# Kernel tuning notes

Hardware: AMD Instinct MI355X
Metric: run time of the kernel (lower is better)

The kernel has to match this reference:

```python
import jax, jax.numpy as jnp
import numpy as np

GROUP_SIZE = 64  # quantization group size along in_features (K)


def setup_inputs() -> dict:
    key = jax.random.key(0)
    k1, k2, k3, k4, k5 = jax.random.split(key, 5)
    M, K, N = 32, 8192, 8192
    num_groups = K // GROUP_SIZE
    x = jax.random.normal(k1, (M, K), dtype=jnp.float32)
    # packed int4 weights: two nibbles per byte along K -> [N, K//2]
    packed_weight = jax.random.randint(k2, (N, K // 2), 0, 256, dtype=jnp.int32)
    scales = jax.random.uniform(k3, (N, num_groups), dtype=jnp.float32) * 0.02 + 1e-3
    zeros = jax.random.uniform(k4, (N, num_groups), dtype=jnp.float32) * 15.0
    bias_param = jax.random.normal(k5, (N,), dtype=jnp.float32)
    return {"x": x, "packed_weight": packed_weight, "scales": scales,
            "zeros": zeros, "bias_param": bias_param}


def reference(x, packed_weight, scales, zeros, bias_param):
    # x: [M, K] float; packed_weight: [N, K//2] int (uint8 semantics)
    # scales/zeros: [N, num_groups]; bias_param: [N]
    K = x.shape[-1]
    k = jnp.arange(K)
    shift = (k % 2) * 4                     # low nibble for even k, high for odd
    # unpack int4: q[n, k] in [0, 15]
    q = (packed_weight[:, k // 2] >> shift[None, :]) & 15   # [N, K]
    gidx = k // GROUP_SIZE                                  # [K]
    # group-wise dequant: (q - zero) * scale
    w = (q.astype(jnp.float32) - zeros[:, gidx]) * scales[:, gidx]  # [N, K]
    out = jnp.einsum('mk,nk->mn', x, w) + bias_param[None, :]        # [M, N]
    return out
```

## Files before the change

### kernel.cpp

```cpp
#include <hip/hip_runtime.h>
#include <hip/hip_bf16.h>


#define KK 8192
#define NN 8192
#define KP 4096
#define NG 128
#define BN 16
#define KSPLIT 2
#define KSW 32
#define NKS 256

typedef __attribute__((ext_vector_type(8))) short short8;
typedef __attribute__((ext_vector_type(4))) float floatx4;

__device__ __forceinline__ unsigned pack_bf16x2(float lo, float hi) {
    union { __hip_bfloat162 h; unsigned u; } c;
    c.h = __float22bfloat162_rn(make_float2(lo, hi));
    return c.u;
}

__global__ void prep_kernel(const float* __restrict__ x, const float* __restrict__ bias,
                            ushort* __restrict__ xb, float* __restrict__ out,
                            int xconv_blocks)
{
    const int bx = blockIdx.x;
    if (bx < xconv_blocks) {
        const int tid = bx * 256 + threadIdx.x;
        const int l   = tid & 63;
        const int ks  = (tid >> 6) & 255;
        const int mt  = tid >> 14;
        const int m   = (l & 15) + 16 * mt;
        const int kb  = ks * 32 + (l >> 4) * 8;
        const float* src = x + (size_t)m * KK + kb;
        const float4 a = *(const float4*)(src);
        const float4 b = *(const float4*)(src + 4);
        *(uint4*)(xb + (size_t)tid * 8) =
            make_uint4(pack_bf16x2(a.x, a.y), pack_bf16x2(a.z, a.w),
                       pack_bf16x2(b.x, b.y), pack_bf16x2(b.z, b.w));
    } else {
        const int f4 = (bx - xconv_blocks) * 256 + threadIdx.x;
        const int n4 = f4 & (NN / 4 - 1);
        const float4 b4 = ((const float4*)bias)[n4];
        ((float4*)out)[f4] = b4;
    }
}

template<bool USE_WS>
__global__ __launch_bounds__(256, 4)
void gptq_mfma_kernel(const int*   __restrict__ pw,
                      const float* __restrict__ scales,
                      const float* __restrict__ zeros,
                      const ushort* __restrict__ xb,
                      const float* __restrict__ x,
                      float* __restrict__ out)
{
    __shared__ float s_lds[64][BN + 1];
    __shared__ float z_lds[64][BN + 1];
    __shared__ float red[4][2][256];

    const int tid  = threadIdx.x;
    const int lane = tid & 63;
    const int wave = tid >> 6;
    const int kh   = blockIdx.x & (KSPLIT - 1);
    const int n0   = (blockIdx.x >> 1) * BN;
    const int g0   = kh * 64;

    {
        const int r  = tid >> 4;
        const int gb = (tid & 15) * 4;
        const float4 s4 = *(const float4*)(scales + (size_t)(n0 + r) * NG + g0 + gb);
        const float4 z4 = *(const float4*)(zeros  + (size_t)(n0 + r) * NG + g0 + gb);
        s_lds[gb + 0][r] = s4.x; s_lds[gb + 1][r] = s4.y;
        s_lds[gb + 2][r] = s4.z; s_lds[gb + 3][r] = s4.w;
        z_lds[gb + 0][r] = z4.x; z_lds[gb + 1][r] = z4.y;
        z_lds[gb + 2][r] = z4.z; z_lds[gb + 3][r] = z4.w;
    }
    __syncthreads();

    const int nl = lane & 15;
    const int kq = lane >> 4;
    const int* pwp = pw + (size_t)(n0 + nl) * KP + kq * 4;
    const uint4* xfp = (const uint4*)xb;
    const int ks0 = kh * 128 + wave * KSW;

    const int xm0 = nl;
    const int xkq = kq * 8;

    auto load_xfrag = [&](int mt, int ks) -> uint4 {
        if (USE_WS) {
            return xfp[(size_t)(mt * NKS + ks) * 64 + lane];
        } else {
            const float* src = x + (size_t)(xm0 + 16 * mt) * KK + ks * 32 + xkq;
            const float4 a = *(const float4*)(src);
            const float4 b = *(const float4*)(src + 4);
            return make_uint4(pack_bf16x2(a.x, a.y), pack_bf16x2(a.z, a.w),
                              pack_bf16x2(b.x, b.y), pack_bf16x2(b.z, b.w));
        }
    };

    floatx4 acc0 = {0.f, 0.f, 0.f, 0.f};
    floatx4 acc1 = {0.f, 0.f, 0.f, 0.f};

    int4  pwb[4];
    uint4 x0b[4], x1b[4];

#pragma unroll
    for (int i = 0; i < 3; ++i) {
        const int ks = ks0 + i;
        pwb[i] = *(const int4*)(pwp + ks * 16);
        x0b[i] = load_xfrag(0, ks);
        x1b[i] = load_xfrag(1, ks);
    }

#pragma unroll 4
    for (int i = 0; i < KSW; ++i) {
        const int slot = i & 3;
        if (i + 3 < KSW) {
            const int ks = ks0 + i + 3;
            const int ps = (i + 3) & 3;
            pwb[ps] = *(const int4*)(pwp + ks * 16);
            x0b[ps] = load_xfrag(0, ks);
            x1b[ps] = load_xfrag(1, ks);
        }
        const int gl  = (wave * KSW + i) >> 1;
        const float sc = s_lds[gl][nl];
        const float zs = -z_lds[gl][nl] * sc;

        union { uint4 v; short8 s; } bf;
        const int4 p = pwb[slot];
        bf.v.x = pack_bf16x2(fmaf((float)(p.x & 15), sc, zs),
                             fmaf((float)((p.x >> 4) & 15), sc, zs));
        bf.v.y = pack_bf16x2(fmaf((float)(p.y & 15), sc, zs),
                             fmaf((float)((p.y >> 4) & 15), sc, zs));
        bf.v.z = pack_bf16x2(fmaf((float)(p.z & 15), sc, zs),
                             fmaf((float)((p.z >> 4) & 15), sc, zs));
        bf.v.w = pack_bf16x2(fmaf((float)(p.w & 15), sc, zs),
                             fmaf((float)((p.w >> 4) & 15), sc, zs));

        union { uint4 v; short8 s; } a0, a1;
        a0.v = x0b[slot];
        a1.v = x1b[slot];
        acc0 = __builtin_amdgcn_mfma_f32_16x16x32_bf16(a0.s, bf.s, acc0, 0, 0, 0);
        acc1 = __builtin_amdgcn_mfma_f32_16x16x32_bf16(a1.s, bf.s, acc1, 0, 0, 0);
    }

#pragma unroll
    for (int r = 0; r < 4; ++r) {
        const int row = kq * 4 + r;
        red[wave][0][row * 16 + nl] = acc0[r];
        red[wave][1][row * 16 + nl] = acc1[r];
    }
    __syncthreads();

#pragma unroll
    for (int i = 0; i < 2; ++i) {
        const int e   = i * 256 + tid;
        const int mt  = e >> 8;
        const int idx = e & 255;
        const float s = red[0][mt][idx] + red[1][mt][idx] + red[2][mt][idx] + red[3][mt][idx];
        const int row = idx >> 4, col = idx & 15;
        atomicAdd(out + (size_t)(mt * 16 + row) * NN + n0 + col, s);
    }
}

extern "C" void kernel_launch(void* const* d_in, const int* in_sizes, int n_in,
                              void* d_out, int out_size, void* d_ws, size_t ws_size,
                              hipStream_t stream) {
    const float* x      = (const float*)d_in[0];
    const int*   pw     = (const int*)  d_in[1];
    const float* scales = (const float*)d_in[2];
    const float* zeros  = (const float*)d_in[3];
    const float* bias   = (const float*)d_in[4];
    float* out = (float*)d_out;

    const size_t need = (size_t)32768 * 16;
    const bool use_ws = (d_ws != nullptr && ws_size >= need);

    if (use_ws) {
        ushort* xb = (ushort*)d_ws;
        prep_kernel<<<128 + 256, 256, 0, stream>>>(x, bias, xb, out, 128);
        gptq_mfma_kernel<true><<<512 * KSPLIT, 256, 0, stream>>>(pw, scales, zeros, xb, x, out);
    } else {
        prep_kernel<<<256, 256, 0, stream>>>(x, bias, nullptr, out, 0);
        gptq_mfma_kernel<false><<<512 * KSPLIT, 256, 0, stream>>>(pw, scales, zeros,
                                                                  (const ushort*)nullptr, x, out);
    }
}
```

Before: 214.6 us.

## Stage weights and activations into LDS via async global_load_lds triple buffering

Replaces the register-prefetch main kernel with one that streams packed weights and bf16 activation fragments into per-wave LDS ring buffers using global_load_lds, with manual vmcnt waits giving a three-deep pipeline. The weight tile is XOR-swizzled to avoid bank conflicts. Scales and zero-offsets now live in registers instead of LDS. A cheaper bit-trick bf16 rounding with v_perm replaces the library pack. The aim is to hide memory latency and free VGPRs, at the cost of lower occupancy (launch bounds 2) and a large LDS footprint.

```diff
diff --git a/kernel.cpp b/kernel.cpp
--- a/kernel.cpp
+++ b/kernel.cpp
@@ -1,5 +1,6 @@
 #include <hip/hip_runtime.h>
 #include <hip/hip_bf16.h>
+#include <stdint.h>
 
 
 #define KK 8192
@@ -10,14 +11,31 @@
 #define KSPLIT 2
 #define KSW 32
 #define NKS 256
+#define NCH 16
+#define BUFB 6144
+#define WREG (3 * BUFB)
 
 typedef __attribute__((ext_vector_type(8))) short short8;
 typedef __attribute__((ext_vector_type(4))) float floatx4;
+typedef const __attribute__((address_space(1))) void* gbl_t;
+typedef __attribute__((address_space(3))) void* lds_t;
+
+__device__ __forceinline__ void async16(const void* g, void* l) {
+    __builtin_amdgcn_global_load_lds((gbl_t)(uintptr_t)g, (lds_t)(uintptr_t)l, 16, 0, 0);
+}
 
 __device__ __forceinline__ unsigned pack_bf16x2(float lo, float hi) {
     union { __hip_bfloat162 h; unsigned u; } c;
     c.h = __float22bfloat162_rn(make_float2(lo, hi));
     return c.u;
+}
+
+__device__ __forceinline__ unsigned dq2(int q, float sc, float zs) {
+    float lo = fmaf((float)(q & 15),        sc, zs);
+    float hi = fmaf((float)((q >> 4) & 15), sc, zs);
+    unsigned ua = __float_as_uint(lo); ua += 0x7fffu + ((ua >> 16) & 1u);
+    unsigned ub = __float_as_uint(hi); ub += 0x7fffu + ((ub >> 16) & 1u);
+    return __builtin_amdgcn_perm(ub, ua, 0x07060302);
 }
 
 __global__ void prep_kernel(const float* __restrict__ x, const float* __restrict__ bias,
@@ -41,19 +59,131 @@
     } else {
         const int f4 = (bx - xconv_blocks) * 256 + threadIdx.x;
         const int n4 = f4 & (NN / 4 - 1);
-        const float4 b4 = ((const float4*)bias)[n4];
-        ((float4*)out)[f4] = b4;
-    }
-}
-
-template<bool USE_WS>
+        ((float4*)out)[f4] = ((const float4*)bias)[n4];
+    }
+}
+
+__global__ __launch_bounds__(256, 2)
+void gptq_mfma_lds(const int*   __restrict__ pw,
+                   const float* __restrict__ scales,
+                   const float* __restrict__ zeros,
+                   const ushort* __restrict__ xb,
+                   float* __restrict__ out)
+{
+    __shared__ uint4 smem4[4 * WREG / 16];
+    uint8_t* smem = (uint8_t*)smem4;
+
+    const int tid  = threadIdx.x;
+    const int lane = tid & 63;
+    const int wave = tid >> 6;
+    const int kh   = blockIdx.x & (KSPLIT - 1);
+    const int n0   = (blockIdx.x >> 1) * BN;
+    const int nl   = lane & 15;
+    const int kq   = lane >> 4;
+    const int ks0  = kh * 128 + wave * KSW;
+    const int g0   = ks0 >> 1;
+
+    float scr[16], zsr[16];
+    {
+        const float* sp = scales + (size_t)(n0 + nl) * NG + g0;
+        const float* zp = zeros  + (size_t)(n0 + nl) * NG + g0;
+#pragma unroll
+        for (int i = 0; i < 4; ++i) {
+            const float4 s4 = *(const float4*)(sp + i * 4);
+            const float4 z4 = *(const float4*)(zp + i * 4);
+            scr[i*4+0] = s4.x; zsr[i*4+0] = -z4.x * s4.x;
+            scr[i*4+1] = s4.y; zsr[i*4+1] = -z4.y * s4.y;
+            scr[i*4+2] = s4.z; zsr[i*4+2] = -z4.z * s4.z;
+            scr[i*4+3] = s4.w; zsr[i*4+3] = -z4.w * s4.w;
+        }
+    }
+
+    const int srow = lane >> 3;
+    const int st   = lane & 7;
+    const int swz  = st ^ srow;
+    const int* pg0 = pw + (size_t)(n0 + 0 + srow) * KP + ks0 * 16 + swz * 4;
+    const int* pg1 = pw + (size_t)(n0 + 8 + srow) * KP + ks0 * 16 + swz * 4;
+    const uint4* xg0 = (const uint4*)xb + (size_t)(0 * NKS + ks0) * 64 + lane;
+    const uint4* xg1 = (const uint4*)xb + (size_t)(1 * NKS + ks0) * 64 + lane;
+
+    uint8_t* wbase = smem + wave * WREG;
+
+#define STAGE(c) do {                                        \
+        uint8_t* b_ = wbase + ((c) % 3) * BUFB;              \
+        async16(pg0 + (c) * 32, b_);                         \
+        async16(pg1 + (c) * 32, b_ + 1024);                  \
+        async16(xg0 + (c) * 128,      b_ + 2048);            \
+        async16(xg0 + (c) * 128 + 64, b_ + 3072);            \
+        async16(xg1 + (c) * 128,      b_ + 4096);            \
+        async16(xg1 + (c) * 128 + 64, b_ + 5120);            \
+    } while (0)
+
+    const int pwo0 = nl * 128 + (((0 * 4 + kq) ^ (nl & 7)) * 16);
+    const int pwo1 = nl * 128 + (((1 * 4 + kq) ^ (nl & 7)) * 16);
+    const int xo   = lane * 16;
+
+    floatx4 acc0 = {0.f, 0.f, 0.f, 0.f};
+    floatx4 acc1 = {0.f, 0.f, 0.f, 0.f};
+
+    STAGE(0);
+    STAGE(1);
+
+#pragma unroll
+    for (int c = 0; c < NCH; ++c) {
+        if (c + 2 < NCH) {
+            STAGE(c + 2);
+            asm volatile("s_waitcnt vmcnt(12)" ::: "memory");
+        } else if (c == NCH - 2) {
+            asm volatile("s_waitcnt vmcnt(6)" ::: "memory");
+        } else {
+            asm volatile("s_waitcnt vmcnt(0)" ::: "memory");
+        }
+        uint8_t* b = wbase + (c % 3) * BUFB;
+        const float sc = scr[c];
+        const float zs = zsr[c];
+#pragma unroll
+        for (int j = 0; j < 2; ++j) {
+            const int4  p  = *(const int4*) (b + (j ? pwo1 : pwo0));
+            union { uint4 v; short8 s; } a0, a1, bf;
+            a0.v = *(const uint4*)(b + 2048 + j * 1024 + xo);
+            a1.v = *(const uint4*)(b + 4096 + j * 1024 + xo);
+            bf.v.x = dq2(p.x, sc, zs);
+            bf.v.y = dq2(p.y, sc, zs);
+            bf.v.z = dq2(p.z, sc, zs);
+            bf.v.w = dq2(p.w, sc, zs);
+            acc0 = __builtin_amdgcn_mfma_f32_16x16x32_bf16(a0.s, bf.s, acc0, 0, 0, 0);
+            acc1 = __builtin_amdgcn_mfma_f32_16x16x32_bf16(a1.s, bf.s, acc1, 0, 0, 0);
+        }
+    }
+#undef STAGE
+
+    __syncthreads();
+    float* red = (float*)smem;
+#pragma unroll
+    for (int r = 0; r < 4; ++r) {
+        const int row = kq * 4 + r;
+        red[(wave * 2 + 0) * 256 + row * 16 + nl] = acc0[r];
+        red[(wave * 2 + 1) * 256 + row * 16 + nl] = acc1[r];
+    }
+    __syncthreads();
+
+#pragma unroll
+    for (int i = 0; i < 2; ++i) {
+        const int e   = i * 256 + tid;
+        const int mt  = e >> 8;
+        const int idx = e & 255;
+        const float s = red[(0 * 2 + mt) * 256 + idx] + red[(1 * 2 + mt) * 256 + idx]
+                      + red[(2 * 2 + mt) * 256 + idx] + red[(3 * 2 + mt) * 256 + idx];
+        atomicAdd(out + (size_t)(mt * 16 + (idx >> 4)) * NN + n0 + (idx & 15), s);
+    }
+}
+
 __global__ __launch_bounds__(256, 4)
-void gptq_mfma_kernel(const int*   __restrict__ pw,
-                      const float* __restrict__ scales,
-                      const float* __restrict__ zeros,
-                      const ushort* __restrict__ xb,
-                      const float* __restrict__ x,
-                      float* __restrict__ out)
+void gptq_mfma_fallback(const int*   __restrict__ pw,
+                        const float* __restrict__ scales,
+                        const float* __restrict__ zeros,
+                        const float* __restrict__ x,
+                        float* __restrict__ out)
 {
     __shared__ float s_lds[64][BN + 1];
     __shared__ float z_lds[64][BN + 1];
@@ -81,27 +211,18 @@
     const int nl = lane & 15;
     const int kq = lane >> 4;
     const int* pwp = pw + (size_t)(n0 + nl) * KP + kq * 4;
-    const uint4* xfp = (const uint4*)xb;
     const int ks0 = kh * 128 + wave * KSW;
 
-    const int xm0 = nl;
-    const int xkq = kq * 8;
-
     auto load_xfrag = [&](int mt, int ks) -> uint4 {
-        if (USE_WS) {
-            return xfp[(size_t)(mt * NKS + ks) * 64 + lane];
-        } else {
-            const float* src = x + (size_t)(xm0 + 16 * mt) * KK + ks * 32 + xkq;
-            const float4 a = *(const float4*)(src);
-            const float4 b = *(const float4*)(src + 4);
-            return make_uint4(pack_bf16x2(a.x, a.y), pack_bf16x2(a.z, a.w),
-                              pack_bf16x2(b.x, b.y), pack_bf16x2(b.z, b.w));
-        }
+        const float* src = x + (size_t)(nl + 16 * mt) * KK + ks * 32 + kq * 8;
+        const float4 a = *(const float4*)(src);
+        const float4 b = *(const float4*)(src + 4);
+        return make_uint4(pack_bf16x2(a.x, a.y), pack_bf16x2(a.z, a.w),
+                          pack_bf16x2(b.x, b.y), pack_bf16x2(b.z, b.w));
     };
 
     floatx4 acc0 = {0.f, 0.f, 0.f, 0.f};
     floatx4 acc1 = {0.f, 0.f, 0.f, 0.f};
-
     int4  pwb[4];
     uint4 x0b[4], x1b[4];
 
@@ -127,18 +248,12 @@
         const float sc = s_lds[gl][nl];
         const float zs = -z_lds[gl][nl] * sc;
 
-        union { uint4 v; short8 s; } bf;
+        union { uint4 v; short8 s; } bf, a0, a1;
         const int4 p = pwb[slot];
-        bf.v.x = pack_bf16x2(fmaf((float)(p.x & 15), sc, zs),
-                             fmaf((float)((p.x >> 4) & 15), sc, zs));
-        bf.v.y = pack_bf16x2(fmaf((float)(p.y & 15), sc, zs),
-                             fmaf((float)((p.y >> 4) & 15), sc, zs));
-        bf.v.z = pack_bf16x2(fmaf((float)(p.z & 15), sc, zs),
-                             fmaf((float)((p.z >> 4) & 15), sc, zs));
-        bf.v.w = pack_bf16x2(fmaf((float)(p.w & 15), sc, zs),
-                             fmaf((float)((p.w >> 4) & 15), sc, zs));
-
-        union { uint4 v; short8 s; } a0, a1;
+        bf.v.x = dq2(p.x, sc, zs);
+        bf.v.y = dq2(p.y, sc, zs);
+        bf.v.z = dq2(p.z, sc, zs);
+        bf.v.w = dq2(p.w, sc, zs);
         a0.v = x0b[slot];
         a1.v = x1b[slot];
         acc0 = __builtin_amdgcn_mfma_f32_16x16x32_bf16(a0.s, bf.s, acc0, 0, 0, 0);
@@ -159,8 +274,7 @@
         const int mt  = e >> 8;
         const int idx = e & 255;
         const float s = red[0][mt][idx] + red[1][mt][idx] + red[2][mt][idx] + red[3][mt][idx];
-        const int row = idx >> 4, col = idx & 15;
-        atomicAdd(out + (size_t)(mt * 16 + row) * NN + n0 + col, s);
+        atomicAdd(out + (size_t)(mt * 16 + (idx >> 4)) * NN + n0 + (idx & 15), s);
     }
 }
 
@@ -175,15 +289,12 @@
     float* out = (float*)d_out;
 
     const size_t need = (size_t)32768 * 16;
-    const bool use_ws = (d_ws != nullptr && ws_size >= need);
-
-    if (use_ws) {
+    if (d_ws != nullptr && ws_size >= need) {
         ushort* xb = (ushort*)d_ws;
         prep_kernel<<<128 + 256, 256, 0, stream>>>(x, bias, xb, out, 128);
-        gptq_mfma_kernel<true><<<512 * KSPLIT, 256, 0, stream>>>(pw, scales, zeros, xb, x, out);
+        gptq_mfma_lds<<<512 * KSPLIT, 256, 0, stream>>>(pw, scales, zeros, xb, out);
     } else {
         prep_kernel<<<256, 256, 0, stream>>>(x, bias, nullptr, out, 0);
-        gptq_mfma_kernel<false><<<512 * KSPLIT, 256, 0, stream>>>(pw, scales, zeros,
-                                                                  (const ushort*)nullptr, x, out);
-    }
-}
+        gptq_mfma_fallback<<<512 * KSPLIT, 256, 0, stream>>>(pw, scales, zeros, x, out);
+    }
+}
```

After: 210.8 us. About the same (-1.8%).
